# Performance work log

Measured on AMD Instinct MI355X. Metric: run time of the kernel, lower is better.

The kernel has to match this reference:

```python
import jax, jax.numpy as jnp
import numpy as np
from jax import lax

# Module hyperparameters (from init_kwargs)
WINDOW_SIZE = 8
STRIDE = 4
BINARY_LEVELS = 8
OUT_DIMS = 8192
M = 64          # number of hash segments
BBITS = 8       # bits per hash
VECTOR_SIZE = OUT_DIMS // M  # 128


def setup_inputs() -> dict:
    key = jax.random.key(0)
    k1, k2 = jax.random.split(key)
    x = jax.random.normal(k1, (256, 3, 224, 224), dtype=jnp.float32)
    R = jax.random.randint(k2, (M, BBITS), 0, 1000, dtype=jnp.int64) if jax.config.jax_enable_x64 else jax.random.randint(k2, (M, BBITS), 0, 1000, dtype=jnp.int32)
    return {"x": x, "R": R}


def reference(x, R):
    b, C, H, W = x.shape
    # --- window striding + per-window max pool (== unfold + adaptive_max_pool(1,1)) ---
    pooled = lax.reduce_window(
        x, -jnp.inf, lax.max,
        window_dimensions=(1, 1, WINDOW_SIZE, WINDOW_SIZE),
        window_strides=(1, 1, STRIDE, STRIDE),
        padding='VALID')                      # [b, C, hp, wp]
    feats = pooled.reshape(b, -1)             # channel-major ordering, matches torch cat over channels

    # --- thermometer binarization (per-row min/max normalize, > thresholds) ---
    x_min = feats.min(axis=1, keepdims=True)
    x_max = feats.max(axis=1, keepdims=True)
    xn = (feats - x_min) / (x_max - x_min + 1e-8)
    thresholds = jnp.linspace(0.0, 1.0, BINARY_LEVELS + 1, dtype=jnp.float32)[1:]
    binarized = (xn[:, :, None] > thresholds[None, None, :]).astype(jnp.float32)  # [b, F, L]

    # --- pseudo-random encoding: gather -> 8-bit hash -> scatter ---
    all_features = binarized.reshape(b, -1)   # [b, n_elements]
    n_elements = all_features.shape[1]
    idx = (R % n_elements).astype(jnp.int32)  # [M, BBITS]
    selected = all_features[:, idx]           # [b, M, BBITS] gather
    weights = (2.0 ** jnp.arange(BBITS - 1, -1, -1)).astype(jnp.float32)
    p = (selected * weights).sum(-1).astype(jnp.int32) % VECTOR_SIZE   # [b, M]
    bit_pos = jnp.arange(M, dtype=jnp.int32)[None, :] * VECTOR_SIZE + p  # [b, M], always < OUT_DIMS
    encoded = jnp.zeros((b, OUT_DIMS), dtype=jnp.float32)
    encoded = encoded.at[jnp.arange(b)[:, None], bit_pos].set(1.0)
    return encoded
```

## Files before the change

### kernel.cpp

```cpp
#include <hip/hip_runtime.h>

#define IH 224
#define IW 224
#define CHW (IH * IW)
#define NCH_CELLS (56 * 56)
#define NCELLS (3 * NCH_CELLS)
#define NP_CELLS (55 * 55)
#define NP_ALL (3 * NP_CELLS)

typedef float fx4 __attribute__((ext_vector_type(4)));

__device__ __forceinline__ fx4 max4(fx4 a, fx4 b) {
  fx4 r;
  r.x = fmaxf(a.x, b.x); r.y = fmaxf(a.y, b.y);
  r.z = fmaxf(a.z, b.z); r.w = fmaxf(a.w, b.w);
  return r;
}

__device__ __forceinline__ float cell_max(const float* __restrict__ p0) {
  fx4 a0 = *reinterpret_cast<const fx4*>(p0);
  fx4 a1 = *reinterpret_cast<const fx4*>(p0 + IW);
  fx4 a2 = *reinterpret_cast<const fx4*>(p0 + 2 * IW);
  fx4 a3 = *reinterpret_cast<const fx4*>(p0 + 3 * IW);
  fx4 mm = max4(max4(a0, a1), max4(a2, a3));
  return fmaxf(fmaxf(mm.x, mm.y), fmaxf(mm.z, mm.w));
}

__device__ __forceinline__ const float* cell_addr(const float* __restrict__ img, int j) {
  const int c  = j / NCH_CELLS;
  const int r  = j - c * NCH_CELLS;
  const int g  = r / 56;
  const int wp = r - g * 56;
  return img + c * CHW + (4 * g) * IW + 4 * wp;
}

__global__ __launch_bounds__(1024, 4) void fused_kernel(
    const float* __restrict__ x,
    const int* __restrict__ R,
    float* __restrict__ out)
{
  __shared__ float gmr[NCELLS];
  __shared__ int   sR[512];
  __shared__ float rmin[16], rmax[16];
  __shared__ float sMin, sMax;

  const int b = blockIdx.x;
  const int t = threadIdx.x;
  const float NEG = -3.4e38f;

  if (t < 512) sR[t] = R[t];

  const float* img = x + (size_t)b * (3 * CHW);

  int j = t;
  for (; j + 1024 < NCELLS; j += 2048) {
    const float* pa = cell_addr(img, j);
    const float* pb = cell_addr(img, j + 1024);
    fx4 a0 = *reinterpret_cast<const fx4*>(pa);
    fx4 a1 = *reinterpret_cast<const fx4*>(pa + IW);
    fx4 a2 = *reinterpret_cast<const fx4*>(pa + 2 * IW);
    fx4 a3 = *reinterpret_cast<const fx4*>(pa + 3 * IW);
    fx4 b0 = *reinterpret_cast<const fx4*>(pb);
    fx4 b1 = *reinterpret_cast<const fx4*>(pb + IW);
    fx4 b2 = *reinterpret_cast<const fx4*>(pb + 2 * IW);
    fx4 b3 = *reinterpret_cast<const fx4*>(pb + 3 * IW);
    fx4 ma = max4(max4(a0, a1), max4(a2, a3));
    fx4 mb = max4(max4(b0, b1), max4(b2, b3));
    gmr[j]        = fmaxf(fmaxf(ma.x, ma.y), fmaxf(ma.z, ma.w));
    gmr[j + 1024] = fmaxf(fmaxf(mb.x, mb.y), fmaxf(mb.z, mb.w));
  }
  for (; j < NCELLS; j += 1024) {
    gmr[j] = cell_max(cell_addr(img, j));
  }
  __syncthreads();

  float lmin = 3.4e38f, lmax = NEG;
  for (int q = t; q < NP_ALL; q += 1024) {
    const int c  = q / NP_CELLS;
    const int r  = q - c * NP_CELLS;
    const int hp = r / 55;
    const int w  = r - hp * 55;
    const float* gp = gmr + c * NCH_CELLS + hp * 56 + w;
    float pm = fmaxf(fmaxf(gp[0], gp[1]), fmaxf(gp[56], gp[57]));
    lmin = fminf(lmin, pm);
    lmax = fmaxf(lmax, pm);
  }
  for (int off = 32; off > 0; off >>= 1) {
    lmin = fminf(lmin, __shfl_down(lmin, off));
    lmax = fmaxf(lmax, __shfl_down(lmax, off));
  }
  if ((t & 63) == 0) { rmin[t >> 6] = lmin; rmax[t >> 6] = lmax; }

  {
    fx4* orow4 = reinterpret_cast<fx4*>(out + (size_t)b * 8192);
    const fx4 z = (fx4)(0.f);
    orow4[t] = z;
    orow4[t + 1024] = z;
  }
  __syncthreads();

  if (t == 0) {
    float mn = rmin[0], mx = rmax[0];
    #pragma unroll
    for (int k = 1; k < 16; ++k) {
      mn = fminf(mn, rmin[k]);
      mx = fmaxf(mx, rmax[k]);
    }
    sMin = mn; sMax = mx;
  }
  __syncthreads();

  if (t < 64) {
    const float xmin  = sMin;
    const float denom = sMax - xmin + 1e-8f;
    int p = 0;
    #pragma unroll
    for (int k = 0; k < 8; ++k) {
      int idx = sR[t * 8 + k] % 72600;
      int f   = idx >> 3;
      int l   = idx & 7;
      int c   = f / NP_CELLS;
      int rem = f - c * NP_CELLS;
      int hp  = rem / 55;
      int w   = rem - hp * 55;
      const float* gp = gmr + c * NCH_CELLS + hp * 56 + w;
      float pm = fmaxf(fmaxf(gp[0], gp[1]), fmaxf(gp[56], gp[57]));
      float xn = (pm - xmin) / denom;
      if (xn > (float)(l + 1) * 0.125f) p += 128 >> k;
    }
    out[(size_t)b * 8192 + t * 128 + (p & 127)] = 1.0f;
  }
}

extern "C" void kernel_launch(void* const* d_in, const int* in_sizes, int n_in,
                              void* d_out, int out_size, void* d_ws, size_t ws_size,
                              hipStream_t stream) {
  const float* x   = (const float*)d_in[0];
  const int*   R   = (const int*)d_in[1];
  float*       out = (float*)d_out;

  fused_kernel<<<256, 1024, 0, stream>>>(x, R, out);
}
```

Measured before the change: 31.11 us.

## Split fused kernel into grid-wide streaming pool pass and per-image tail kernel

```diff
diff --git a/kernel.cpp b/kernel.cpp
--- a/kernel.cpp
+++ b/kernel.cpp
@@ -7,6 +7,7 @@
 #define NCELLS (3 * NCH_CELLS)
 #define NP_CELLS (55 * 55)
 #define NP_ALL (3 * NP_CELLS)
+#define TOTCELLS (256 * NCELLS)
 
 typedef float fx4 __attribute__((ext_vector_type(4)));
 
@@ -15,6 +16,16 @@
   r.x = fmaxf(a.x, b.x); r.y = fmaxf(a.y, b.y);
   r.z = fmaxf(a.z, b.z); r.w = fmaxf(a.w, b.w);
   return r;
+}
+
+__device__ __forceinline__ const float* cell_addr(const float* __restrict__ x, int J) {
+  const int b  = J / NCELLS;
+  const int j  = J - b * NCELLS;
+  const int c  = j / NCH_CELLS;
+  const int r  = j - c * NCH_CELLS;
+  const int g  = r / 56;
+  const int wp = r - g * 56;
+  return x + (size_t)b * (3 * CHW) + c * CHW + (4 * g) * IW + 4 * wp;
 }
 
 __device__ __forceinline__ float cell_max(const float* __restrict__ p0) {
@@ -26,7 +37,117 @@
   return fmaxf(fmaxf(mm.x, mm.y), fmaxf(mm.z, mm.w));
 }
 
-__device__ __forceinline__ const float* cell_addr(const float* __restrict__ img, int j) {
+__global__ __launch_bounds__(256) void stream_kernel(
+    const float* __restrict__ x,
+    float* __restrict__ gmr_g)
+{
+  int J = blockIdx.x * 256 + threadIdx.x;
+  const int STRIDE = 2048 * 256;
+  for (; J + STRIDE < TOTCELLS; J += 2 * STRIDE) {
+    const float* pa = cell_addr(x, J);
+    const float* pb = cell_addr(x, J + STRIDE);
+    fx4 a0 = *reinterpret_cast<const fx4*>(pa);
+    fx4 a1 = *reinterpret_cast<const fx4*>(pa + IW);
+    fx4 a2 = *reinterpret_cast<const fx4*>(pa + 2 * IW);
+    fx4 a3 = *reinterpret_cast<const fx4*>(pa + 3 * IW);
+    fx4 b0 = *reinterpret_cast<const fx4*>(pb);
+    fx4 b1 = *reinterpret_cast<const fx4*>(pb + IW);
+    fx4 b2 = *reinterpret_cast<const fx4*>(pb + 2 * IW);
+    fx4 b3 = *reinterpret_cast<const fx4*>(pb + 3 * IW);
+    fx4 ma = max4(max4(a0, a1), max4(a2, a3));
+    fx4 mb = max4(max4(b0, b1), max4(b2, b3));
+    gmr_g[J]          = fmaxf(fmaxf(ma.x, ma.y), fmaxf(ma.z, ma.w));
+    gmr_g[J + STRIDE] = fmaxf(fmaxf(mb.x, mb.y), fmaxf(mb.z, mb.w));
+  }
+  for (; J < TOTCELLS; J += STRIDE) {
+    gmr_g[J] = cell_max(cell_addr(x, J));
+  }
+}
+
+__global__ __launch_bounds__(1024, 4) void tail_kernel(
+    const float* __restrict__ gmr_g,
+    const int* __restrict__ R,
+    float* __restrict__ out)
+{
+  __shared__ float gmr[NCELLS];
+  __shared__ int   sR[512];
+  __shared__ float rmin[16], rmax[16];
+  __shared__ float sMin, sMax;
+
+  const int b = blockIdx.x;
+  const int t = threadIdx.x;
+  const float NEG = -3.4e38f;
+
+  if (t < 512) sR[t] = R[t];
+
+  {
+    const fx4* src = reinterpret_cast<const fx4*>(gmr_g + (size_t)b * NCELLS);
+    fx4* dst = reinterpret_cast<fx4*>(gmr);
+    dst[t] = src[t];
+    dst[t + 1024] = src[t + 1024];
+    if (t < 2352 - 2048) dst[t + 2048] = src[t + 2048];
+  }
+  __syncthreads();
+
+  float lmin = 3.4e38f, lmax = NEG;
+  for (int q = t; q < NP_ALL; q += 1024) {
+    const int c  = q / NP_CELLS;
+    const int r  = q - c * NP_CELLS;
+    const int hp = r / 55;
+    const int w  = r - hp * 55;
+    const float* gp = gmr + c * NCH_CELLS + hp * 56 + w;
+    float pm = fmaxf(fmaxf(gp[0], gp[1]), fmaxf(gp[56], gp[57]));
+    lmin = fminf(lmin, pm);
+    lmax = fmaxf(lmax, pm);
+  }
+  for (int off = 32; off > 0; off >>= 1) {
+    lmin = fminf(lmin, __shfl_down(lmin, off));
+    lmax = fmaxf(lmax, __shfl_down(lmax, off));
+  }
+  if ((t & 63) == 0) { rmin[t >> 6] = lmin; rmax[t >> 6] = lmax; }
+
+  {
+    fx4* orow4 = reinterpret_cast<fx4*>(out + (size_t)b * 8192);
+    const fx4 z = (fx4)(0.f);
+    orow4[t] = z;
+    orow4[t + 1024] = z;
+  }
+  __syncthreads();
+
+  if (t == 0) {
+    float mn = rmin[0], mx = rmax[0];
+    #pragma unroll
+    for (int k = 1; k < 16; ++k) {
+      mn = fminf(mn, rmin[k]);
+      mx = fmaxf(mx, rmax[k]);
+    }
+    sMin = mn; sMax = mx;
+  }
+  __syncthreads();
+
+  if (t < 64) {
+    const float xmin  = sMin;
+    const float denom = sMax - xmin + 1e-8f;
+    int p = 0;
+    #pragma unroll
+    for (int k = 0; k < 8; ++k) {
+      int idx = sR[t * 8 + k] % 72600;
+      int f   = idx >> 3;
+      int l   = idx & 7;
+      int c   = f / NP_CELLS;
+      int rem = f - c * NP_CELLS;
+      int hp  = rem / 55;
+      int w   = rem - hp * 55;
+      const float* gp = gmr + c * NCH_CELLS + hp * 56 + w;
+      float pm = fmaxf(fmaxf(gp[0], gp[1]), fmaxf(gp[56], gp[57]));
+      float xn = (pm - xmin) / denom;
+      if (xn > (float)(l + 1) * 0.125f) p += 128 >> k;
+    }
+    out[(size_t)b * 8192 + t * 128 + (p & 127)] = 1.0f;
+  }
+}
+
+__device__ __forceinline__ const float* cell_addr1(const float* __restrict__ img, int j) {
   const int c  = j / NCH_CELLS;
   const int r  = j - c * NCH_CELLS;
   const int g  = r / 56;
@@ -54,8 +175,8 @@
 
   int j = t;
   for (; j + 1024 < NCELLS; j += 2048) {
-    const float* pa = cell_addr(img, j);
-    const float* pb = cell_addr(img, j + 1024);
+    const float* pa = cell_addr1(img, j);
+    const float* pb = cell_addr1(img, j + 1024);
     fx4 a0 = *reinterpret_cast<const fx4*>(pa);
     fx4 a1 = *reinterpret_cast<const fx4*>(pa + IW);
     fx4 a2 = *reinterpret_cast<const fx4*>(pa + 2 * IW);
@@ -70,7 +191,7 @@
     gmr[j + 1024] = fmaxf(fmaxf(mb.x, mb.y), fmaxf(mb.z, mb.w));
   }
   for (; j < NCELLS; j += 1024) {
-    gmr[j] = cell_max(cell_addr(img, j));
+    gmr[j] = cell_max(cell_addr1(img, j));
   }
   __syncthreads();
 
@@ -139,5 +260,11 @@
   const int*   R   = (const int*)d_in[1];
   float*       out = (float*)d_out;
 
-  fused_kernel<<<256, 1024, 0, stream>>>(x, R, out);
-}
+  if (ws_size >= (size_t)TOTCELLS * sizeof(float)) {
+    float* gmr_g = (float*)d_ws;
+    stream_kernel<<<2048, 256, 0, stream>>>(x, gmr_g);
+    tail_kernel<<<256, 1024, 0, stream>>>(gmr_g, R, out);
+  } else {
+    fused_kernel<<<256, 1024, 0, stream>>>(x, R, out);
+  }
+}
```

Result: slower. 36.55 us (+17.5%).
